# Kernel tuning notes

Hardware: AMD Instinct MI355X
Metric: run time of the kernel (lower is better)

Reference implementation:

```python
import jax, jax.numpy as jnp
import numpy as np

N = 50000       # nodes
D = 256         # in_features == out_features
G = 4           # feature groups / adjacencies
E = 800000      # edges per group (avg degree 16)


def setup_inputs() -> dict:
    key = jax.random.key(0)
    k1, k2, k3, k4, k5, k6 = jax.random.split(key, 6)
    x = jax.random.normal(k1, (N, D), dtype=jnp.float32)
    edge_row = jax.random.randint(k2, (G, E), 0, N, dtype=jnp.int32)
    edge_col = jax.random.randint(k3, (G, E), 0, N, dtype=jnp.int32)
    edge_val = jax.random.uniform(k4, (G, E), dtype=jnp.float32)
    stdv = 1.0 / np.sqrt(D)
    weight = jax.random.normal(k5, (D, D), dtype=jnp.float32) * stdv
    bias = jax.random.normal(k6, (D,), dtype=jnp.float32) * stdv
    return {"x": x, "edge_row": edge_row, "edge_col": edge_col,
            "edge_val": edge_val, "weight": weight, "bias": bias}


def reference(x, edge_row, edge_col, edge_val, weight, bias):
    n, d = x.shape
    g = edge_row.shape[0]
    dg = d // g
    # [G, N, dg]: contiguous column blocks per group
    xg = x.reshape(n, g, dg).transpose(1, 0, 2)

    def spmm(xb, row, col, val):
        # out[r] += val * xb[c]  (reduce='add' SpMM)
        msg = val[:, None] * xb[col]          # [E, dg]
        return jax.ops.segment_sum(msg, row, num_segments=n)

    outs = jax.vmap(spmm)(xg, edge_row, edge_col, edge_val)  # [G, N, dg]
    outputs = outs.transpose(1, 0, 2).reshape(n, d)           # [N, D]
    return outputs @ weight + bias
```

## Files before the change

kernel.cpp:

```cpp
#include <hip/hip_runtime.h>
#include <hip/hip_bf16.h>

#define N_NODES 50000
#define D_FEAT  256
#define G_GROUPS 4
#define E_EDGES 800000
#define DG      64
#define M_SEG   (G_GROUPS * N_NODES)
#define TOT_E   (G_GROUPS * E_EDGES)
#define M_PAD   50048

#define SEGB      256
#define NB1       782
#define CAP       4608
#define LDSE      4872
#define CA_BLOCKS 400
#define CHA       8000
#define CHG       (CHA / 4)

#define PREP_CVX  1563
#define PREP_CW   64
#define PREP_TOT  (PREP_CVX + PREP_CW)

typedef short bf16x8 __attribute__((ext_vector_type(8)));
typedef float f32x4  __attribute__((ext_vector_type(4)));

__device__ __forceinline__ unsigned short f2bf(float f) {
    unsigned int u = __float_as_uint(f);
    u += 0x7FFF + ((u >> 16) & 1);
    return (unsigned short)(u >> 16);
}
__device__ __forceinline__ float bf2f(unsigned short h) {
    return __uint_as_float((unsigned int)h << 16);
}

__global__ __launch_bounds__(1024) void prep_kernel(
    const float* __restrict__ x, unsigned short* __restrict__ xb,
    const float* __restrict__ W, unsigned short* __restrict__ Wt)
{
    const int b = blockIdx.x, t = threadIdx.x;
    if (b < PREP_CVX) {
        const long long base = ((long long)b * 1024 + t) * 8;
        if (base < (long long)N_NODES * D_FEAT) {
            const float4 v0 = *(const float4*)&x[base];
            const float4 v1 = *(const float4*)&x[base + 4];
            unsigned short r[8];
            r[0] = f2bf(v0.x); r[1] = f2bf(v0.y); r[2] = f2bf(v0.z); r[3] = f2bf(v0.w);
            r[4] = f2bf(v1.x); r[5] = f2bf(v1.y); r[6] = f2bf(v1.z); r[7] = f2bf(v1.w);
            *(uint4*)&xb[base] = *(const uint4*)r;
        }
        return;
    }
    const int idx = (b - PREP_CVX) * 1024 + t;
    const int n = idx >> 8, k = idx & 255;
    Wt[n * D_FEAT + k] = f2bf(W[k * D_FEAT + n]);
}

__global__ __launch_bounds__(1024) void scatterA_kernel(
    const int* __restrict__ edge_row, const int* __restrict__ edge_col,
    const float* __restrict__ edge_val, int* __restrict__ bcnt,
    int2* __restrict__ epA)
{
    __shared__ int hist[NB1];
    __shared__ int gcur[NB1];
    const int t = threadIdx.x;
    if (t < NB1) hist[t] = 0;
    __syncthreads();
    const int start = blockIdx.x * CHA;
    const int segbase = (start / E_EDGES) * N_NODES;
    const bool hasB = (t + 1024) < CHG;

    const int4 ra = *(const int4*)&edge_row[start + 4 * t];
    int4 rb = make_int4(0, 0, 0, 0);
    if (hasB) rb = *(const int4*)&edge_row[start + 4 * (t + 1024)];
    const int sA0 = segbase + ra.x, sA1 = segbase + ra.y;
    const int sA2 = segbase + ra.z, sA3 = segbase + ra.w;
    atomicAdd(&hist[sA0 >> 8], 1);
    atomicAdd(&hist[sA1 >> 8], 1);
    atomicAdd(&hist[sA2 >> 8], 1);
    atomicAdd(&hist[sA3 >> 8], 1);
    int sB0 = 0, sB1 = 0, sB2 = 0, sB3 = 0;
    if (hasB) {
        sB0 = segbase + rb.x; sB1 = segbase + rb.y;
        sB2 = segbase + rb.z; sB3 = segbase + rb.w;
        atomicAdd(&hist[sB0 >> 8], 1);
        atomicAdd(&hist[sB1 >> 8], 1);
        atomicAdd(&hist[sB2 >> 8], 1);
        atomicAdd(&hist[sB3 >> 8], 1);
    }
    __syncthreads();
    if (t < NB1) gcur[t] = hist[t] ? atomicAdd(&bcnt[t], hist[t]) : 0;
    __syncthreads();

#define SCAT(sv, cc, vv)                                             \
    {                                                                \
        const int bk = (sv) >> 8;                                    \
        const int rel = atomicAdd(&gcur[bk], 1);                     \
        if (rel < CAP)                                               \
            epA[bk * CAP + rel] =                                    \
                make_int2((cc) | (((sv) & (SEGB - 1)) << 16), (vv)); \
    }
    {
        const int4 c = *(const int4*)&edge_col[start + 4 * t];
        const int4 v = *(const int4*)&((const int*)edge_val)[start + 4 * t];
        SCAT(sA0, c.x, v.x) SCAT(sA1, c.y, v.y)
        SCAT(sA2, c.z, v.z) SCAT(sA3, c.w, v.w)
    }
    if (hasB) {
        const int4 c = *(const int4*)&edge_col[start + 4 * (t + 1024)];
        const int4 v = *(const int4*)&((const int*)edge_val)[start + 4 * (t + 1024)];
        SCAT(sB0, c.x, v.x) SCAT(sB1, c.y, v.y)
        SCAT(sB2, c.z, v.z) SCAT(sB3, c.w, v.w)
    }
#undef SCAT
}

__global__ __launch_bounds__(512) void sort_spmm_kernel(
    const unsigned short* __restrict__ xb, const int2* __restrict__ epA,
    const int* __restrict__ bcnt, unsigned short* __restrict__ tmpb)
{
    __shared__ int2 eplds[LDSE];
    __shared__ int hist[SEGB];
    __shared__ int lofs[SEGB];
    __shared__ int cur[SEGB];
    __shared__ int ssum[SEGB];
    const int b = blockIdx.x, t = threadIdx.x;
    const int rb = b * CAP;
    const int n = min(bcnt[b], CAP);
    const int seg0 = b * SEGB;
    const int g0 = seg0 / N_NODES;
    const int bnd = (g0 + 1) * N_NODES;

    for (int i = t; i < LDSE; i += 512) eplds[i] = make_int2(0, 0);
    if (t < SEGB) hist[t] = 0;
    __syncthreads();
    for (int j = t; j < n; j += 512)
        atomicAdd(&hist[((unsigned)epA[rb + j].x) >> 16], 1);
    __syncthreads();
    int pc = 0;
    if (t < SEGB) { pc = (hist[t] + 1) & ~1; ssum[t] = pc; }
    __syncthreads();
    for (int off = 1; off < SEGB; off <<= 1) {
        int add = 0;
        if (t < SEGB && t >= off) add = ssum[t - off];
        __syncthreads();
        if (t < SEGB) ssum[t] += add;
        __syncthreads();
    }
    if (t < SEGB) { const int eb = ssum[t] - pc; lofs[t] = eb; cur[t] = eb; }
    __syncthreads();
    for (int j = t; j < n; j += 512) {
        const int2 p = epA[rb + j];
        const int sl = ((unsigned)p.x) >> 16;
        const int col = p.x & 0xFFFF;
        const int gg = (seg0 + sl >= bnd) ? (g0 + 1) : g0;
        const int pos = atomicAdd(&cur[sl], 1);
        eplds[pos] = make_int2((col << 9) | (gg << 7), p.y);
    }
    __syncthreads();

    const int nseg = min(SEGB, M_SEG - seg0);
    const int wv = t >> 6, tl = t & 63;
    const int o = tl >> 3, ls = tl & 7;
    const char* __restrict__ xbb = (const char*)xb + ls * 16;

#define ACC8(v, r)                                          \
    a0 = fmaf(v, __uint_as_float((r).x << 16), a0);         \
    a1 = fmaf(v, __uint_as_float((r).x & 0xFFFF0000u), a1); \
    a2 = fmaf(v, __uint_as_float((r).y << 16), a2);         \
    a3 = fmaf(v, __uint_as_float((r).y & 0xFFFF0000u), a3); \
    a4 = fmaf(v, __uint_as_float((r).z << 16), a4);         \
    a5 = fmaf(v, __uint_as_float((r).z & 0xFFFF0000u), a5); \
    a6 = fmaf(v, __uint_as_float((r).w << 16), a6);         \
    a7 = fmaf(v, __uint_as_float((r).w & 0xFFFF0000u), a7);

    #pragma unroll 1
    for (int r = 0; r < 4; ++r) {
        const int sl = r * 64 + wv * 8 + o;
        const bool act = sl < nseg;
        int j = act ? lofs[sl] : 0;
        const int ep_ = act ? (j + ((hist[sl] + 1) & ~1)) : 0;
        const int emax2 = (ep_ - 2 > j) ? (ep_ - 2) : j;

        float a0 = 0.f, a1 = 0.f, a2 = 0.f, a3 = 0.f;
        float a4 = 0.f, a5 = 0.f, a6 = 0.f, a7 = 0.f;

        while (__ballot(j < ep_)) {
            const int jc0 = min(j, emax2);
            const int jc1 = min(j + 2, emax2);
            const int4 q0 = *(const int4*)&eplds[jc0];
            const int4 q1 = *(const int4*)&eplds[jc1];
            const uint4 r0 = *(const uint4*)(xbb + q0.x);
            const uint4 r1 = *(const uint4*)(xbb + q0.z);
            const uint4 r2 = *(const uint4*)(xbb + q1.x);
            const uint4 r3 = *(const uint4*)(xbb + q1.z);
            const bool cA = j < ep_;
            const bool cB = (j + 2) < ep_;
            const float v0 = cA ? __int_as_float(q0.y) : 0.f;
            const float v1 = cA ? __int_as_float(q0.w) : 0.f;
            const float v2 = cB ? __int_as_float(q1.y) : 0.f;
            const float v3 = cB ? __int_as_float(q1.w) : 0.f;
            ACC8(v0, r0)
            ACC8(v1, r1)
            ACC8(v2, r2)
            ACC8(v3, r3)
            j += 4;
        }
        if (act) {
            const int seg = seg0 + sl;
            const int g = (seg >= bnd) ? (g0 + 1) : g0;
            const int row = seg - g * N_NODES;
            const unsigned o0w = (unsigned)f2bf(a0) | ((unsigned)f2bf(a1) << 16);
            const unsigned o1w = (unsigned)f2bf(a2) | ((unsigned)f2bf(a3) << 16);
            const unsigned o2w = (unsigned)f2bf(a4) | ((unsigned)f2bf(a5) << 16);
            const unsigned o3w = (unsigned)f2bf(a6) | ((unsigned)f2bf(a7) << 16);
            *(uint4*)((char*)tmpb + (size_t)row * 512 + g * 128 + ls * 16) =
                make_uint4(o0w, o1w, o2w, o3w);
        }
    }
#undef ACC8
}

#define TBK 32
#define LDP 40

__global__ __launch_bounds__(256) void gemm_mfma_kernel(
    const unsigned short* __restrict__ A, const unsigned short* __restrict__ Bt,
    const float* __restrict__ bias, float* __restrict__ C)
{
    __shared__ unsigned short As[128][LDP];
    __shared__ unsigned short Bs[128][LDP];

    const int tid = threadIdx.x;
    const int wid = tid >> 6, lane = tid & 63;
    const int wm = (wid & 1) * 64, wn = (wid >> 1) * 64;
    const int lm = lane & 15, lq = lane >> 4;
    const int row0 = blockIdx.x * 128, col0 = blockIdx.y * 128;

    f32x4 acc[4][4] = {};

    for (int k0 = 0; k0 < D_FEAT; k0 += TBK) {
        #pragma unroll
        for (int l = 0; l < 2; ++l) {
            const int chunk = tid + l * 256;
            const int r = chunk >> 2;
            const int c = (chunk & 3) * 8;
            uint4 v = make_uint4(0u, 0u, 0u, 0u);
            const int gr = row0 + r;
            if (gr < N_NODES)
                v = *(const uint4*)&A[(long long)gr * D_FEAT + k0 + c];
            *(uint4*)&As[r][c] = v;
        }
        #pragma unroll
        for (int l = 0; l < 2; ++l) {
            const int chunk = tid + l * 256;
            const int r = chunk >> 2;
            const int c = (chunk & 3) * 8;
            *(uint4*)&Bs[r][c] =
                *(const uint4*)&Bt[(long long)(col0 + r) * D_FEAT + k0 + c];
        }
        __syncthreads();

        bf16x8 af[4], bfr[4];
        #pragma unroll
        for (int mi = 0; mi < 4; ++mi)
            af[mi] = *(const bf16x8*)&As[wm + mi * 16 + lm][lq * 8];
        #pragma unroll
        for (int ni = 0; ni < 4; ++ni)
            bfr[ni] = *(const bf16x8*)&Bs[wn + ni * 16 + lm][lq * 8];
        #pragma unroll
        for (int mi = 0; mi < 4; ++mi)
            #pragma unroll
            for (int ni = 0; ni < 4; ++ni)
                acc[mi][ni] = __builtin_amdgcn_mfma_f32_16x16x32_bf16(
                    af[mi], bfr[ni], acc[mi][ni], 0, 0, 0);
        __syncthreads();
    }

    #pragma unroll
    for (int mi = 0; mi < 4; ++mi) {
        #pragma unroll
        for (int ni = 0; ni < 4; ++ni) {
            const int n = col0 + wn + ni * 16 + lm;
            const float b = bias[n];
            #pragma unroll
            for (int r = 0; r < 4; ++r) {
                const int m = row0 + wm + mi * 16 + lq * 4 + r;
                if (m < N_NODES)
                    C[(long long)m * D_FEAT + n] = acc[mi][ni][r] + b;
            }
        }
    }
}

__global__ __launch_bounds__(256) void spmm_scatter_kernel(
    const float* __restrict__ x, const int* __restrict__ edge_row,
    const int* __restrict__ edge_col, const float* __restrict__ edge_val,
    float* __restrict__ tmp)
{
    const long long gtid = (long long)blockIdx.x * blockDim.x + threadIdx.x;
    const int wave = (int)(gtid >> 6);
    const int lane = threadIdx.x & 63;
    if (wave >= TOT_E) return;
    const int g = wave / E_EDGES;
    const int row = edge_row[wave];
    const int col = edge_col[wave];
    const float val = edge_val[wave];
    atomicAdd(&tmp[(long long)row * D_FEAT + g * DG + lane],
              val * x[(long long)col * D_FEAT + g * DG + lane]);
}

__global__ __launch_bounds__(256) void gemm_bias_kernel(
    const float* __restrict__ A, const float* __restrict__ W,
    const float* __restrict__ bias, float* __restrict__ C)
{
    __shared__ float Asf[64][68];
    __shared__ float Wsf[64][68];
    const int tid = threadIdx.x;
    const int tx = tid & 15, ty = tid >> 4;
    const int row0 = blockIdx.x * 64, col0 = blockIdx.y * 64;
    float acc[4][4] = {};
    for (int k0 = 0; k0 < D_FEAT; k0 += 64) {
        #pragma unroll
        for (int l = 0; l < 4; ++l) {
            const int linear = tid + l * 256;
            const int ar = linear >> 4, ac = (linear & 15) << 2;
            float4 v = make_float4(0.f, 0.f, 0.f, 0.f);
            const int gr = row0 + ar;
            if (gr < N_NODES) v = *(const float4*)&A[(long long)gr * D_FEAT + k0 + ac];
            Asf[ac + 0][ar] = v.x; Asf[ac + 1][ar] = v.y;
            Asf[ac + 2][ar] = v.z; Asf[ac + 3][ar] = v.w;
        }
        #pragma unroll
        for (int l = 0; l < 4; ++l) {
            const int linear = tid + l * 256;
            const int wr = linear >> 4, wc = (linear & 15) << 2;
            *(float4*)&Wsf[wr][wc] =
                *(const float4*)&W[(long long)(k0 + wr) * D_FEAT + col0 + wc];
        }
        __syncthreads();
        #pragma unroll
        for (int k = 0; k < 64; ++k) {
            const float4 a4 = *(const float4*)&Asf[k][ty * 4];
            const float4 b4 = *(const float4*)&Wsf[k][tx * 4];
            const float a[4] = {a4.x, a4.y, a4.z, a4.w};
            const float b[4] = {b4.x, b4.y, b4.z, b4.w};
            #pragma unroll
            for (int i = 0; i < 4; ++i)
                #pragma unroll
                for (int j = 0; j < 4; ++j) acc[i][j] += a[i] * b[j];
        }
        __syncthreads();
    }
    const float4 b4 = *(const float4*)&bias[col0 + tx * 4];
    #pragma unroll
    for (int i = 0; i < 4; ++i) {
        const int gr = row0 + ty * 4 + i;
        if (gr >= N_NODES) continue;
        float4 v;
        v.x = acc[i][0] + b4.x; v.y = acc[i][1] + b4.y;
        v.z = acc[i][2] + b4.z; v.w = acc[i][3] + b4.w;
        *(float4*)&C[(long long)gr * D_FEAT + col0 + tx * 4] = v;
    }
}

extern "C" void kernel_launch(void* const* d_in, const int* in_sizes, int n_in,
                              void* d_out, int out_size, void* d_ws, size_t ws_size,
                              hipStream_t stream)
{
    const float* x        = (const float*)d_in[0];
    const int*   edge_row = (const int*)d_in[1];
    const int*   edge_col = (const int*)d_in[2];
    const float* edge_val = (const float*)d_in[3];
    const float* weight   = (const float*)d_in[4];
    const float* bias     = (const float*)d_in[5];
    float* out = (float*)d_out;

    char* p = (char*)d_ws;
    auto alloc = [&](size_t bytes) {
        char* r = p;
        p += (bytes + 255) & ~(size_t)255;
        return r;
    };
    unsigned short* xb   = (unsigned short*)alloc((size_t)N_NODES * D_FEAT * 2);
    unsigned short* tmpb = (unsigned short*)alloc((size_t)M_PAD * D_FEAT * 2);
    unsigned short* Wt   = (unsigned short*)alloc((size_t)D_FEAT * D_FEAT * 2);
    int2* epA = (int2*)alloc((size_t)NB1 * CAP * sizeof(int2));
    int* bcnt = (int*)alloc((size_t)NB1 * sizeof(int));
    const size_t needed = (size_t)(p - (char*)d_ws);

    if (ws_size >= needed) {
        hipMemsetAsync(bcnt, 0, (size_t)NB1 * sizeof(int), stream);
        prep_kernel<<<PREP_TOT, 1024, 0, stream>>>(x, xb, weight, Wt);
        scatterA_kernel<<<CA_BLOCKS, 1024, 0, stream>>>(
            edge_row, edge_col, edge_val, bcnt, epA);
        sort_spmm_kernel<<<NB1, 512, 0, stream>>>(xb, epA, bcnt, tmpb);
        dim3 grid(M_PAD / 128, D_FEAT / 128);
        gemm_mfma_kernel<<<grid, 256, 0, stream>>>(tmpb, Wt, bias, out);
    } else {
        float* tmp = (float*)d_ws;
        hipMemsetAsync(tmp, 0, (size_t)N_NODES * D_FEAT * sizeof(float), stream);
        const long long total_threads = (long long)TOT_E * 64;
        spmm_scatter_kernel<<<(int)((total_threads + 255) / 256), 256, 0, stream>>>(
            x, edge_row, edge_col, edge_val, tmp);
        dim3 grid2((N_NODES + 63) / 64, D_FEAT / 64);
        gemm_bias_kernel<<<grid2, 256, 0, stream>>>(tmp, weight, bias, out);
    }
}
```

Before: 272.5 us.

## Fuse scatter and prep kernels, halve segment bucket size to 128

Merges the x/W bf16 conversion kernel and the edge bucketing scatter kernel into one launch, with scatter blocks first and prep blocks after, so the two independent jobs share the GPU and one launch is saved. It also halves the row-segment bucket size from 256 to 128, doubling the bucket count and the number of sort/SpMM blocks while shrinking per-block LDS capacity. This should raise parallelism and occupancy in the SpMM stage, at the cost of more global bucket atomics and a larger histogram per scatter block. It also brings a higher risk of bucket overflow because the per-bucket capacity is smaller.

```diff
diff --git a/kernel.cpp b/kernel.cpp
--- a/kernel.cpp
+++ b/kernel.cpp
@@ -10,17 +10,17 @@
 #define TOT_E   (G_GROUPS * E_EDGES)
 #define M_PAD   50048
 
-#define SEGB      256
-#define NB1       782
-#define CAP       4608
-#define LDSE      4872
-#define CA_BLOCKS 400
+#define SEGB      128
+#define NB1       1563
+#define CAP       2432
+#define LDSE      2568
+#define SC_BLKS   400
 #define CHA       8000
 #define CHG       (CHA / 4)
 
 #define PREP_CVX  1563
 #define PREP_CW   64
-#define PREP_TOT  (PREP_CVX + PREP_CW)
+#define FUSED_TOT (SC_BLKS + PREP_CVX + PREP_CW)
 
 typedef short bf16x8 __attribute__((ext_vector_type(8)));
 typedef float f32x4  __attribute__((ext_vector_type(4)));
@@ -34,39 +34,42 @@
     return __uint_as_float((unsigned int)h << 16);
 }
 
-__global__ __launch_bounds__(1024) void prep_kernel(
+__global__ __launch_bounds__(1024) void fused_scatter_prep_kernel(
+    const int* __restrict__ edge_row, const int* __restrict__ edge_col,
+    const float* __restrict__ edge_val, int* __restrict__ bcnt,
+    int2* __restrict__ epA,
     const float* __restrict__ x, unsigned short* __restrict__ xb,
     const float* __restrict__ W, unsigned short* __restrict__ Wt)
 {
-    const int b = blockIdx.x, t = threadIdx.x;
-    if (b < PREP_CVX) {
-        const long long base = ((long long)b * 1024 + t) * 8;
-        if (base < (long long)N_NODES * D_FEAT) {
-            const float4 v0 = *(const float4*)&x[base];
-            const float4 v1 = *(const float4*)&x[base + 4];
-            unsigned short r[8];
-            r[0] = f2bf(v0.x); r[1] = f2bf(v0.y); r[2] = f2bf(v0.z); r[3] = f2bf(v0.w);
-            r[4] = f2bf(v1.x); r[5] = f2bf(v1.y); r[6] = f2bf(v1.z); r[7] = f2bf(v1.w);
-            *(uint4*)&xb[base] = *(const uint4*)r;
-        }
-        return;
-    }
-    const int idx = (b - PREP_CVX) * 1024 + t;
-    const int n = idx >> 8, k = idx & 255;
-    Wt[n * D_FEAT + k] = f2bf(W[k * D_FEAT + n]);
-}
-
-__global__ __launch_bounds__(1024) void scatterA_kernel(
-    const int* __restrict__ edge_row, const int* __restrict__ edge_col,
-    const float* __restrict__ edge_val, int* __restrict__ bcnt,
-    int2* __restrict__ epA)
-{
     __shared__ int hist[NB1];
     __shared__ int gcur[NB1];
-    const int t = threadIdx.x;
-    if (t < NB1) hist[t] = 0;
-    __syncthreads();
-    const int start = blockIdx.x * CHA;
+    const int b = blockIdx.x, t = threadIdx.x;
+
+    if (b >= SC_BLKS) {
+        const int pb = b - SC_BLKS;
+        if (pb < PREP_CVX) {
+            const long long base = ((long long)pb * 1024 + t) * 8;
+            if (base < (long long)N_NODES * D_FEAT) {
+                const float4 v0 = *(const float4*)&x[base];
+                const float4 v1 = *(const float4*)&x[base + 4];
+                unsigned short r[8];
+                r[0] = f2bf(v0.x); r[1] = f2bf(v0.y);
+                r[2] = f2bf(v0.z); r[3] = f2bf(v0.w);
+                r[4] = f2bf(v1.x); r[5] = f2bf(v1.y);
+                r[6] = f2bf(v1.z); r[7] = f2bf(v1.w);
+                *(uint4*)&xb[base] = *(const uint4*)r;
+            }
+        } else {
+            const int idx = (pb - PREP_CVX) * 1024 + t;
+            const int n = idx >> 8, k = idx & 255;
+            Wt[n * D_FEAT + k] = f2bf(W[k * D_FEAT + n]);
+        }
+        return;
+    }
+
+    for (int i = t; i < NB1; i += 1024) hist[i] = 0;
+    __syncthreads();
+    const int start = b * CHA;
     const int segbase = (start / E_EDGES) * N_NODES;
     const bool hasB = (t + 1024) < CHG;
 
@@ -75,26 +78,27 @@
     if (hasB) rb = *(const int4*)&edge_row[start + 4 * (t + 1024)];
     const int sA0 = segbase + ra.x, sA1 = segbase + ra.y;
     const int sA2 = segbase + ra.z, sA3 = segbase + ra.w;
-    atomicAdd(&hist[sA0 >> 8], 1);
-    atomicAdd(&hist[sA1 >> 8], 1);
-    atomicAdd(&hist[sA2 >> 8], 1);
-    atomicAdd(&hist[sA3 >> 8], 1);
+    atomicAdd(&hist[sA0 >> 7], 1);
+    atomicAdd(&hist[sA1 >> 7], 1);
+    atomicAdd(&hist[sA2 >> 7], 1);
+    atomicAdd(&hist[sA3 >> 7], 1);
     int sB0 = 0, sB1 = 0, sB2 = 0, sB3 = 0;
     if (hasB) {
         sB0 = segbase + rb.x; sB1 = segbase + rb.y;
         sB2 = segbase + rb.z; sB3 = segbase + rb.w;
-        atomicAdd(&hist[sB0 >> 8], 1);
-        atomicAdd(&hist[sB1 >> 8], 1);
-        atomicAdd(&hist[sB2 >> 8], 1);
-        atomicAdd(&hist[sB3 >> 8], 1);
-    }
-    __syncthreads();
-    if (t < NB1) gcur[t] = hist[t] ? atomicAdd(&bcnt[t], hist[t]) : 0;
+        atomicAdd(&hist[sB0 >> 7], 1);
+        atomicAdd(&hist[sB1 >> 7], 1);
+        atomicAdd(&hist[sB2 >> 7], 1);
+        atomicAdd(&hist[sB3 >> 7], 1);
+    }
+    __syncthreads();
+    for (int i = t; i < NB1; i += 1024)
+        gcur[i] = hist[i] ? atomicAdd(&bcnt[i], hist[i]) : 0;
     __syncthreads();
 
 #define SCAT(sv, cc, vv)                                             \
     {                                                                \
-        const int bk = (sv) >> 8;                                    \
+        const int bk = (sv) >> 7;                                    \
         const int rel = atomicAdd(&gcur[bk], 1);                     \
         if (rel < CAP)                                               \
             epA[bk * CAP + rel] =                                    \
@@ -175,7 +179,7 @@
     a7 = fmaf(v, __uint_as_float((r).w & 0xFFFF0000u), a7);
 
     #pragma unroll 1
-    for (int r = 0; r < 4; ++r) {
+    for (int r = 0; r < 2; ++r) {
         const int sl = r * 64 + wv * 8 + o;
         const bool act = sl < nseg;
         int j = act ? lofs[sl] : 0;
@@ -391,9 +395,8 @@
 
     if (ws_size >= needed) {
         hipMemsetAsync(bcnt, 0, (size_t)NB1 * sizeof(int), stream);
-        prep_kernel<<<PREP_TOT, 1024, 0, stream>>>(x, xb, weight, Wt);
-        scatterA_kernel<<<CA_BLOCKS, 1024, 0, stream>>>(
-            edge_row, edge_col, edge_val, bcnt, epA);
+        fused_scatter_prep_kernel<<<FUSED_TOT, 1024, 0, stream>>>(
+            edge_row, edge_col, edge_val, bcnt, epA, x, xb, weight, Wt);
         sort_spmm_kernel<<<NB1, 512, 0, stream>>>(xb, epA, bcnt, tmpb);
         dim3 grid(M_PAD / 128, D_FEAT / 128);
         gemm_mfma_kernel<<<grid, 256, 0, stream>>>(tmpb, Wt, bias, out);
```

New measurement: 245.7 us. -9.8%, faster.
